# Performance work log

Hardware: AMD Instinct MI355X
Metric: run time of the kernel (lower is better)

Reference implementation:

```python
import jax, jax.numpy as jnp
import numpy as np

MARGIN = 0.3
NEG_FILL = 1000000.0


def setup_inputs() -> dict:
    key = jax.random.key(0)
    k1, k2 = jax.random.split(key)
    features = jax.random.normal(k1, (8192, 128), dtype=jnp.float32)
    labels = jax.random.randint(k2, (8192,), 0, 512, dtype=jnp.int64)
    return {"features": features, "labels": labels}


def _triplet_loss(features, labels):
    N = features.shape[0]
    # pairwise euclidean distances via gram trick (matches torch.cdist p=2)
    sq = jnp.sum(features * features, axis=1)               # [N]
    d2 = sq[:, None] + sq[None, :] - 2.0 * (features @ features.T)
    d2 = jnp.maximum(d2, 0.0)
    # guard sqrt(0) on diagonal for clean gradients
    dist = jnp.where(d2 > 0.0, jnp.sqrt(jnp.where(d2 > 0.0, d2, 1.0)), 0.0)  # [N,N]

    same = labels[:, None] == labels[None, :]
    eye = jnp.eye(N, dtype=bool)
    is_pos = same & ~eye
    is_neg = ~same

    neg_inf = jnp.float32(-jnp.inf)
    pos_inf = jnp.float32(jnp.inf)
    has_pos = jnp.any(is_pos, axis=1)
    has_neg = jnp.any(is_neg, axis=1)
    # hardest positive: masked row max; empty -> 0.0
    dist_ap = jnp.max(jnp.where(is_pos, dist, neg_inf), axis=1)
    dist_ap = jnp.where(has_pos, dist_ap, 0.0)
    # hardest negative: masked row min; empty -> 1e6
    dist_an = jnp.min(jnp.where(is_neg, dist, pos_inf), axis=1)
    dist_an = jnp.where(has_neg, dist_an, NEG_FILL)

    # MarginRankingLoss with y=1: mean(max(0, margin - (dist_an - dist_ap)))
    return jnp.mean(jnp.maximum(0.0, MARGIN - (dist_an - dist_ap)))


def reference(features, labels):
    return _triplet_loss(features, labels)
```

## Files before the change

### kernel.cpp

```cpp
#include <hip/hip_runtime.h>
#include <hip/hip_bf16.h>
#include <math.h>

#define N 8192
#define D 128
#define MARGIN_V 0.3f
#define NEG_FILL 1000000.0f

typedef short bf16x8 __attribute__((ext_vector_type(8)));
typedef float f32x4  __attribute__((ext_vector_type(4)));

__device__ __forceinline__ void g2l16(const void* g, void* l) {
    __builtin_amdgcn_global_load_lds(
        (const __attribute__((address_space(1))) void*)g,
        (__attribute__((address_space(3))) void*)l, 16, 0, 0);
}

__global__ __launch_bounds__(256) void convert_kernel(const float* __restrict__ F,
                                                      unsigned short* __restrict__ Fb,
                                                      float* __restrict__ sq,
                                                      unsigned* __restrict__ ap,
                                                      unsigned* __restrict__ an) {
    int row  = blockIdx.x * 4 + (threadIdx.x >> 6);
    int lane = threadIdx.x & 63;
    float2 v = *(const float2*)&F[row * D + lane * 2];
    float s = v.x * v.x + v.y * v.y;
    __hip_bfloat162 t = __float22bfloat162_rn(v);
    *(unsigned int*)&Fb[row * D + lane * 2] = *(unsigned int*)&t;
    #pragma unroll
    for (int off = 32; off >= 1; off >>= 1) s += __shfl_xor(s, off);
    if (lane == 0) sq[row] = s;
    int gid = blockIdx.x * 256 + threadIdx.x;
    if (gid < N) { ap[gid] = 0u; an[gid] = 0x7F800000u; }
}

__global__ __launch_bounds__(256, 2) void gemm_kernel(const unsigned short* __restrict__ Fb,
                                                      const float* __restrict__ sq,
                                                      const int* __restrict__ lab,
                                                      unsigned* __restrict__ ap,
                                                      unsigned* __restrict__ an) {
    __shared__ __align__(16) unsigned short As[128 * 128];
    __shared__ __align__(16) unsigned short Bs[2][64 * 128];
    __shared__ float sqj_s[1024];
    __shared__ int   labj_s[1024];
    __shared__ float sqi_s[128];
    __shared__ int   labi_s[128];

    const int bi = blockIdx.x & 63;
    const int jc = blockIdx.x >> 6;
    const int i0 = bi * 128;
    const int jbase0 = jc * 1024;
    const int tid  = threadIdx.x;
    const int wave = tid >> 6, lane = tid & 63;
    const int wy = wave >> 1, wx = wave & 1;
    const int quad = lane >> 4, lr = lane & 15;

    {
        f32x4 v = *(const f32x4*)&sq[jbase0 + tid * 4];
        *(f32x4*)&sqj_s[tid * 4] = v;
        int4 w4 = *(const int4*)&lab[jbase0 + tid * 4];
        *(int4*)&labj_s[tid * 4] = w4;
    }
    if (tid < 128) { sqi_s[tid] = sq[i0 + tid]; labi_s[tid] = lab[i0 + tid]; }

    #pragma unroll
    for (int it = 0; it < 8; ++it) {
        int c_id = it * 256 + tid;
        int row = c_id >> 4, p = c_id & 15;
        int sc = (p & 8) | ((p ^ row) & 7);
        g2l16(Fb + (size_t)(i0 + row) * D + sc * 8, (char*)As + c_id * 16);
    }
    #pragma unroll
    for (int it = 0; it < 4; ++it) {
        int c_id = it * 256 + tid;
        int row = c_id >> 4, p = c_id & 15;
        int sc = (p & 8) | ((p ^ row) & 7);
        g2l16(Fb + (size_t)(jbase0 + row) * D + sc * 8, (char*)&Bs[0][0] + c_id * 16);
    }
    __syncthreads();

    bf16x8 af[4][4];
    #pragma unroll
    for (int a = 0; a < 4; ++a)
        #pragma unroll
        for (int ks = 0; ks < 4; ++ks) {
            int row = wy * 64 + a * 16 + lr;
            int kc  = ks * 4 + quad;
            int pos = (kc & 8) | ((kc ^ row) & 7);
            af[a][ks] = *(const bf16x8*)&As[row * 128 + pos * 8];
        }
    f32x4 sqi4[4]; int4 labi4[4];
    #pragma unroll
    for (int a = 0; a < 4; ++a) {
        int base = wy * 64 + a * 16 + quad * 4;
        sqi4[a]  = *(const f32x4*)&sqi_s[base];
        labi4[a] = *(const int4*)&labi_s[base];
    }

    float rowP[4][4], rowN[4][4];
    #pragma unroll
    for (int a = 0; a < 4; ++a)
        #pragma unroll
        for (int r = 0; r < 4; ++r) { rowP[a][r] = -INFINITY; rowN[a][r] = INFINITY; }

    #pragma unroll 2
    for (int t = 0; t < 16; ++t) {
        if (t < 15) {
            #pragma unroll
            for (int it = 0; it < 4; ++it) {
                int c_id = it * 256 + tid;
                int row = c_id >> 4, p = c_id & 15;
                int sc = (p & 8) | ((p ^ row) & 7);
                g2l16(Fb + (size_t)(jbase0 + (t + 1) * 64 + row) * D + sc * 8,
                      (char*)&Bs[(t + 1) & 1][0] + c_id * 16);
            }
        }
        float sqj_l[2]; int labj_l[2];
        #pragma unroll
        for (int b = 0; b < 2; ++b) {
            int cl = t * 64 + wx * 32 + b * 16 + lr;
            sqj_l[b]  = sqj_s[cl];
            labj_l[b] = labj_s[cl];
        }
        f32x4 acc[4][2];
        #pragma unroll
        for (int a = 0; a < 4; ++a)
            #pragma unroll
            for (int b = 0; b < 2; ++b) acc[a][b] = {0.f, 0.f, 0.f, 0.f};
        #pragma unroll
        for (int ks = 0; ks < 4; ++ks) {
            bf16x8 bfr[2];
            #pragma unroll
            for (int b = 0; b < 2; ++b) {
                int rb  = wx * 32 + b * 16 + lr;
                int kc  = ks * 4 + quad;
                int pos = (kc & 8) | ((kc ^ rb) & 7);
                bfr[b] = *(const bf16x8*)&Bs[t & 1][rb * 128 + pos * 8];
            }
            #pragma unroll
            for (int a = 0; a < 4; ++a)
                #pragma unroll
                for (int b = 0; b < 2; ++b)
                    acc[a][b] = __builtin_amdgcn_mfma_f32_16x16x32_bf16(af[a][ks], bfr[b], acc[a][b], 0, 0, 0);
        }
        __syncthreads();

        #pragma unroll
        for (int a = 0; a < 4; ++a)
            #pragma unroll
            for (int b = 0; b < 2; ++b)
                #pragma unroll
                for (int r = 0; r < 4; ++r) {
                    float u = fmaf(acc[a][b][r], -2.0f, sqj_l[b]);
                    bool same = (labi4[a][r] == labj_l[b]);
                    rowP[a][r] = fmaxf(rowP[a][r], same ? u : -INFINITY);
                    rowN[a][r] = fminf(rowN[a][r], same ? INFINITY : u);
                }
    }

    #pragma unroll
    for (int a = 0; a < 4; ++a)
        #pragma unroll
        for (int r = 0; r < 4; ++r) {
            float p = rowP[a][r], n = rowN[a][r];
            #pragma unroll
            for (int off = 1; off < 16; off <<= 1) {
                p = fmaxf(p, __shfl_xor(p, off));
                n = fminf(n, __shfl_xor(n, off));
            }
            rowP[a][r] = p; rowN[a][r] = n;
        }
    if (lr == 0) {
        #pragma unroll
        for (int a = 0; a < 4; ++a)
            #pragma unroll
            for (int r = 0; r < 4; ++r) {
                int row = i0 + wy * 64 + a * 16 + quad * 4 + r;
                float pd2 = fmaxf(sqi4[a][r] + rowP[a][r], 0.f);
                float nd2 = fmaxf(sqi4[a][r] + rowN[a][r], 0.f);
                atomicMax(&ap[row], __float_as_uint(pd2));
                atomicMin(&an[row], __float_as_uint(nd2));
            }
    }
}

__global__ __launch_bounds__(256) void loss_kernel(const float* __restrict__ ap,
                                                   const float* __restrict__ an,
                                                   float* __restrict__ out) {
    int tid = threadIdx.x;
    float sum = 0.f;
    #pragma unroll
    for (int k = 0; k < 8; ++k) {
        int i = k * 1024 + tid * 4;
        f32x4 a4 = *(const f32x4*)&ap[i];
        f32x4 n4 = *(const f32x4*)&an[i];
        #pragma unroll
        for (int c = 0; c < 4; ++c) {
            float apd = __builtin_amdgcn_sqrtf(a4[c]);
            float anv = n4[c];
            float and_ = (anv < INFINITY) ? __builtin_amdgcn_sqrtf(anv) : NEG_FILL;
            sum += fmaxf(0.f, MARGIN_V - (and_ - apd));
        }
    }
    #pragma unroll
    for (int off = 32; off >= 1; off >>= 1) sum += __shfl_xor(sum, off);
    __shared__ float s4[4];
    if ((tid & 63) == 0) s4[tid >> 6] = sum;
    __syncthreads();
    if (tid == 0) out[0] = (s4[0] + s4[1] + s4[2] + s4[3]) * (1.0f / (float)N);
}

extern "C" void kernel_launch(void* const* d_in, const int* in_sizes, int n_in,
                              void* d_out, int out_size, void* d_ws, size_t ws_size,
                              hipStream_t stream) {
    const float* F   = (const float*)d_in[0];
    const int*   lab = (const int*)d_in[1];

    unsigned short* Fb = (unsigned short*)d_ws;
    float*          sq = (float*)(Fb + (size_t)N * D);
    unsigned*       ap = (unsigned*)(sq + N);
    unsigned*       an = ap + N;

    convert_kernel<<<N / 4, 256, 0, stream>>>(F, Fb, sq, ap, an);
    gemm_kernel<<<512, 256, 0, stream>>>(Fb, sq, lab, ap, an);
    loss_kernel<<<1, 256, 0, stream>>>((const float*)ap, (const float*)an, (float*)d_out);
}
```

Before: 86.56 us.

## Load B fragments directly from global into registers, drop LDS staging

Replaces the LDS double-buffered B tile (async global-to-LDS loads plus a per-tile barrier) with direct per-lane global loads of MFMA B fragments into registers, software-pipelined across two register buffers. This removes the __syncthreads per tile and the LDS round trip, and frees LDS, which may allow higher occupancy. In exchange, each wave loads its own B rows with no sharing across the wy waves, so global/L2 traffic doubles, and the register footprint grows.

Result: slower. 94.71 us (+9.4%).

```diff
diff --git a/kernel.cpp b/kernel.cpp
--- a/kernel.cpp
+++ b/kernel.cpp
@@ -40,7 +40,6 @@
                                                       unsigned* __restrict__ ap,
                                                       unsigned* __restrict__ an) {
     __shared__ __align__(16) unsigned short As[128 * 128];
-    __shared__ __align__(16) unsigned short Bs[2][64 * 128];
     __shared__ float sqj_s[1024];
     __shared__ int   labj_s[1024];
     __shared__ float sqi_s[128];
@@ -70,13 +69,6 @@
         int sc = (p & 8) | ((p ^ row) & 7);
         g2l16(Fb + (size_t)(i0 + row) * D + sc * 8, (char*)As + c_id * 16);
     }
-    #pragma unroll
-    for (int it = 0; it < 4; ++it) {
-        int c_id = it * 256 + tid;
-        int row = c_id >> 4, p = c_id & 15;
-        int sc = (p & 8) | ((p ^ row) & 7);
-        g2l16(Fb + (size_t)(jbase0 + row) * D + sc * 8, (char*)&Bs[0][0] + c_id * 16);
-    }
     __syncthreads();
 
     bf16x8 af[4][4];
@@ -103,60 +95,66 @@
         #pragma unroll
         for (int r = 0; r < 4; ++r) { rowP[a][r] = -INFINITY; rowN[a][r] = INFINITY; }
 
-    #pragma unroll 2
-    for (int t = 0; t < 16; ++t) {
-        if (t < 15) {
-            #pragma unroll
-            for (int it = 0; it < 4; ++it) {
-                int c_id = it * 256 + tid;
-                int row = c_id >> 4, p = c_id & 15;
-                int sc = (p & 8) | ((p ^ row) & 7);
-                g2l16(Fb + (size_t)(jbase0 + (t + 1) * 64 + row) * D + sc * 8,
-                      (char*)&Bs[(t + 1) & 1][0] + c_id * 16);
-            }
-        }
-        float sqj_l[2]; int labj_l[2];
-        #pragma unroll
-        for (int b = 0; b < 2; ++b) {
-            int cl = t * 64 + wx * 32 + b * 16 + lr;
-            sqj_l[b]  = sqj_s[cl];
-            labj_l[b] = labj_s[cl];
-        }
-        f32x4 acc[4][2];
-        #pragma unroll
-        for (int a = 0; a < 4; ++a)
-            #pragma unroll
-            for (int b = 0; b < 2; ++b) acc[a][b] = {0.f, 0.f, 0.f, 0.f};
-        #pragma unroll
-        for (int ks = 0; ks < 4; ++ks) {
-            bf16x8 bfr[2];
-            #pragma unroll
-            for (int b = 0; b < 2; ++b) {
-                int rb  = wx * 32 + b * 16 + lr;
-                int kc  = ks * 4 + quad;
-                int pos = (kc & 8) | ((kc ^ rb) & 7);
-                bfr[b] = *(const bf16x8*)&Bs[t & 1][rb * 128 + pos * 8];
-            }
-            #pragma unroll
-            for (int a = 0; a < 4; ++a)
-                #pragma unroll
-                for (int b = 0; b < 2; ++b)
-                    acc[a][b] = __builtin_amdgcn_mfma_f32_16x16x32_bf16(af[a][ks], bfr[b], acc[a][b], 0, 0, 0);
-        }
-        __syncthreads();
-
-        #pragma unroll
-        for (int a = 0; a < 4; ++a)
-            #pragma unroll
-            for (int b = 0; b < 2; ++b)
-                #pragma unroll
-                for (int r = 0; r < 4; ++r) {
-                    float u = fmaf(acc[a][b][r], -2.0f, sqj_l[b]);
-                    bool same = (labi4[a][r] == labj_l[b]);
-                    rowP[a][r] = fmaxf(rowP[a][r], same ? u : -INFINITY);
-                    rowN[a][r] = fminf(rowN[a][r], same ? INFINITY : u);
-                }
-    }
+    const unsigned short* Bp = Fb + (size_t)(jbase0 + wx * 32 + lr) * D + quad * 8;
+    const int c0 = wx * 32 + lr;
+
+#define LOAD_BTILE(T, DST)                                                      \
+    {                                                                           \
+        _Pragma("unroll")                                                       \
+        for (int b = 0; b < 2; ++b) {                                           \
+            const unsigned short* p_ = Bp + (size_t)((T) * 64 + b * 16) * D;    \
+            _Pragma("unroll")                                                   \
+            for (int ks = 0; ks < 4; ++ks)                                      \
+                DST[b][ks] = *(const bf16x8*)(p_ + ks * 32);                    \
+        }                                                                       \
+    }
+
+#define COMPUTE_TILE(T, BFR)                                                    \
+    {                                                                           \
+        float sqj_l[2]; int labj_l[2];                                          \
+        _Pragma("unroll")                                                       \
+        for (int b = 0; b < 2; ++b) {                                           \
+            int cl = (T) * 64 + c0 + b * 16;                                    \
+            sqj_l[b]  = sqj_s[cl];                                              \
+            labj_l[b] = labj_s[cl];                                             \
+        }                                                                       \
+        f32x4 acc[4][2];                                                        \
+        _Pragma("unroll")                                                       \
+        for (int a = 0; a < 4; ++a)                                             \
+            _Pragma("unroll")                                                   \
+            for (int b = 0; b < 2; ++b) acc[a][b] = {0.f, 0.f, 0.f, 0.f};       \
+        _Pragma("unroll")                                                       \
+        for (int ks = 0; ks < 4; ++ks)                                          \
+            _Pragma("unroll")                                                   \
+            for (int a = 0; a < 4; ++a)                                         \
+                _Pragma("unroll")                                               \
+                for (int b = 0; b < 2; ++b)                                     \
+                    acc[a][b] = __builtin_amdgcn_mfma_f32_16x16x32_bf16(        \
+                        af[a][ks], BFR[b][ks], acc[a][b], 0, 0, 0);             \
+        _Pragma("unroll")                                                       \
+        for (int a = 0; a < 4; ++a)                                             \
+            _Pragma("unroll")                                                   \
+            for (int b = 0; b < 2; ++b)                                         \
+                _Pragma("unroll")                                               \
+                for (int r = 0; r < 4; ++r) {                                   \
+                    float u = fmaf(acc[a][b][r], -2.0f, sqj_l[b]);              \
+                    bool same = (labi4[a][r] == labj_l[b]);                     \
+                    rowP[a][r] = fmaxf(rowP[a][r], same ? u : -INFINITY);       \
+                    rowN[a][r] = fminf(rowN[a][r], same ? INFINITY : u);        \
+                }                                                               \
+    }
+
+    bf16x8 bf0[2][4], bf1[2][4];
+    LOAD_BTILE(0, bf0);
+    #pragma unroll 1
+    for (int t = 0; t < 16; t += 2) {
+        LOAD_BTILE(t + 1, bf1);
+        COMPUTE_TILE(t, bf0);
+        if (t + 2 < 16) LOAD_BTILE(t + 2, bf0);
+        COMPUTE_TILE(t + 1, bf1);
+    }
+#undef LOAD_BTILE
+#undef COMPUTE_TILE
 
     #pragma unroll
     for (int a = 0; a < 4; ++a)
```

## Exploit distance symmetry to compute only upper-triangular tiles with column reductions

Applied to the files above, without the earlier changes.

Remaps the grid so each block processes only tiles on or above the diagonal of the pairwise distance matrix. Each tile now also reduces per-column hardest positive/negative values through shared memory and updates those rows with atomics. This roughly halves the MFMA and epilogue work, at the cost of extra column reductions, more atomics and uneven block lengths.

Result: slower. 94.97 us (+9.7%).

```diff
diff --git a/kernel.cpp b/kernel.cpp
--- a/kernel.cpp
+++ b/kernel.cpp
@@ -41,25 +41,28 @@
                                                       unsigned* __restrict__ an) {
     __shared__ __align__(16) unsigned short As[128 * 128];
     __shared__ __align__(16) unsigned short Bs[2][64 * 128];
-    __shared__ float sqj_s[1024];
-    __shared__ int   labj_s[1024];
+    __shared__ float sqj_s[512];
+    __shared__ int   labj_s[512];
     __shared__ float sqi_s[128];
     __shared__ int   labi_s[128];
 
-    const int bi = blockIdx.x & 63;
-    const int jc = blockIdx.x >> 6;
-    const int i0 = bi * 128;
-    const int jbase0 = jc * 1024;
+    int k = blockIdx.x;
+    int s = 0, cum = 0;
+    while (true) { int cnt = 16 - (s >> 2); if (k < cum + cnt) break; cum += cnt; ++s; }
+    int c = (s >> 2) + (k - cum);
+    int t0 = 2 * s - 8 * c; if (t0 < 0) t0 = 0;
+
+    const int i0 = s * 128, j0 = c * 512;
     const int tid  = threadIdx.x;
     const int wave = tid >> 6, lane = tid & 63;
     const int wy = wave >> 1, wx = wave & 1;
     const int quad = lane >> 4, lr = lane & 15;
 
     {
-        f32x4 v = *(const f32x4*)&sq[jbase0 + tid * 4];
-        *(f32x4*)&sqj_s[tid * 4] = v;
-        int4 w4 = *(const int4*)&lab[jbase0 + tid * 4];
-        *(int4*)&labj_s[tid * 4] = w4;
+        float2 v = *(const float2*)&sq[j0 + tid * 2];
+        sqj_s[tid * 2] = v.x; sqj_s[tid * 2 + 1] = v.y;
+        int2 w = *(const int2*)&lab[j0 + tid * 2];
+        labj_s[tid * 2] = w.x; labj_s[tid * 2 + 1] = w.y;
     }
     if (tid < 128) { sqi_s[tid] = sq[i0 + tid]; labi_s[tid] = lab[i0 + tid]; }
 
@@ -75,7 +78,7 @@
         int c_id = it * 256 + tid;
         int row = c_id >> 4, p = c_id & 15;
         int sc = (p & 8) | ((p ^ row) & 7);
-        g2l16(Fb + (size_t)(jbase0 + row) * D + sc * 8, (char*)&Bs[0][0] + c_id * 16);
+        g2l16(Fb + (size_t)(j0 + t0 * 64 + row) * D + sc * 8, (char*)&Bs[0][0] + c_id * 16);
     }
     __syncthreads();
 
@@ -96,6 +99,12 @@
         sqi4[a]  = *(const f32x4*)&sqi_s[base];
         labi4[a] = *(const int4*)&labi_s[base];
     }
+    __syncthreads();
+
+    float* colP_s = (float*)As;
+    float* colN_s = (float*)As + 1024;
+    ((f32x4*)colP_s)[tid] = {-INFINITY, -INFINITY, -INFINITY, -INFINITY};
+    ((f32x4*)colN_s)[tid] = { INFINITY,  INFINITY,  INFINITY,  INFINITY};
 
     float rowP[4][4], rowN[4][4];
     #pragma unroll
@@ -103,22 +112,22 @@
         #pragma unroll
         for (int r = 0; r < 4; ++r) { rowP[a][r] = -INFINITY; rowN[a][r] = INFINITY; }
 
-    #pragma unroll 2
-    for (int t = 0; t < 16; ++t) {
-        if (t < 15) {
+    #pragma unroll 1
+    for (int t = t0; t < 8; ++t) {
+        if (t < 7) {
             #pragma unroll
             for (int it = 0; it < 4; ++it) {
                 int c_id = it * 256 + tid;
                 int row = c_id >> 4, p = c_id & 15;
                 int sc = (p & 8) | ((p ^ row) & 7);
-                g2l16(Fb + (size_t)(jbase0 + (t + 1) * 64 + row) * D + sc * 8,
+                g2l16(Fb + (size_t)(j0 + (t + 1) * 64 + row) * D + sc * 8,
                       (char*)&Bs[(t + 1) & 1][0] + c_id * 16);
             }
         }
         float sqj_l[2]; int labj_l[2];
         #pragma unroll
         for (int b = 0; b < 2; ++b) {
-            int cl = t * 64 + wx * 32 + b * 16 + lr;
+            int cl = (t << 6) + wx * 32 + b * 16 + lr;
             sqj_l[b]  = sqj_s[cl];
             labj_l[b] = labj_s[cl];
         }
@@ -145,18 +154,40 @@
         }
         __syncthreads();
 
+        float colP[2] = {-INFINITY, -INFINITY}, colN[2] = {INFINITY, INFINITY};
         #pragma unroll
         for (int a = 0; a < 4; ++a)
             #pragma unroll
             for (int b = 0; b < 2; ++b)
                 #pragma unroll
                 for (int r = 0; r < 4; ++r) {
-                    float u = fmaf(acc[a][b][r], -2.0f, sqj_l[b]);
+                    float u  = fmaf(acc[a][b][r], -2.0f, sqj_l[b]);
+                    float d2 = u + sqi4[a][r];
                     bool same = (labi4[a][r] == labj_l[b]);
-                    rowP[a][r] = fmaxf(rowP[a][r], same ? u : -INFINITY);
-                    rowN[a][r] = fminf(rowN[a][r], same ? INFINITY : u);
+                    float pv = same ? d2 : -INFINITY;
+                    float nv = same ? INFINITY : d2;
+                    rowP[a][r] = fmaxf(rowP[a][r], pv);
+                    rowN[a][r] = fminf(rowN[a][r], nv);
+                    colP[b] = fmaxf(colP[b], pv);
+                    colN[b] = fminf(colN[b], nv);
                 }
-    }
+        #pragma unroll
+        for (int b = 0; b < 2; ++b) {
+            colP[b] = fmaxf(colP[b], __shfl_xor(colP[b], 16));
+            colP[b] = fmaxf(colP[b], __shfl_xor(colP[b], 32));
+            colN[b] = fminf(colN[b], __shfl_xor(colN[b], 16));
+            colN[b] = fminf(colN[b], __shfl_xor(colN[b], 32));
+        }
+        if (quad == 0) {
+            #pragma unroll
+            for (int b = 0; b < 2; ++b) {
+                int col = (t << 6) + wx * 32 + b * 16 + lr;
+                colP_s[wy * 512 + col] = colP[b];
+                colN_s[wy * 512 + col] = colN[b];
+            }
+        }
+    }
+    __syncthreads();
 
     #pragma unroll
     for (int a = 0; a < 4; ++a)
@@ -176,11 +207,17 @@
             #pragma unroll
             for (int r = 0; r < 4; ++r) {
                 int row = i0 + wy * 64 + a * 16 + quad * 4 + r;
-                float pd2 = fmaxf(sqi4[a][r] + rowP[a][r], 0.f);
-                float nd2 = fmaxf(sqi4[a][r] + rowN[a][r], 0.f);
-                atomicMax(&ap[row], __float_as_uint(pd2));
-                atomicMin(&an[row], __float_as_uint(nd2));
-            }
+                atomicMax(&ap[row], __float_as_uint(fmaxf(rowP[a][r], 0.f)));
+                atomicMin(&an[row], __float_as_uint(fmaxf(rowN[a][r], 0.f)));
+            }
+    }
+    for (int jj = tid; jj < 512; jj += 256) {
+        if ((jj >> 6) >= t0) {
+            float P = fmaxf(colP_s[jj], colP_s[512 + jj]);
+            float Nv = fminf(colN_s[jj], colN_s[512 + jj]);
+            atomicMax(&ap[j0 + jj], __float_as_uint(fmaxf(P, 0.f)));
+            atomicMin(&an[j0 + jj], __float_as_uint(fmaxf(Nv, 0.f)));
+        }
     }
 }
 
@@ -222,6 +259,6 @@
     unsigned*       an = ap + N;
 
     convert_kernel<<<N / 4, 256, 0, stream>>>(F, Fb, sq, ap, an);
-    gemm_kernel<<<512, 256, 0, stream>>>(Fb, sq, lab, ap, an);
+    gemm_kernel<<<544, 256, 0, stream>>>(Fb, sq, lab, ap, an);
     loss_kernel<<<1, 256, 0, stream>>>((const float*)ap, (const float*)an, (float*)d_out);
 }
```
